# Kernel tuning notes

Measured on AMD Instinct MI355X. Metric: run time of the kernel, lower is better.

Reference implementation:

```python
import jax, jax.numpy as jnp
import numpy as np

NUM_CLASSES = 50000
FEAT_DIM = 256
BATCH = 131072
LAMBDA_CENT = 0.5
EPS = 1e-12  # matches F.normalize default eps


def setup_inputs() -> dict:
    key = jax.random.key(0)
    k1, k2, k3 = jax.random.split(key, 3)
    features = jax.random.normal(k1, (BATCH, FEAT_DIM), dtype=jnp.float32)
    labels = jax.random.randint(k2, (BATCH,), 0, NUM_CLASSES)
    centers = jax.random.normal(k3, (NUM_CLASSES, FEAT_DIM), dtype=jnp.float32)
    return {"features": features, "labels": labels, "centers": centers}


def reference(features, labels, centers):
    # L2 normalize rows (F.normalize, p=2, dim=1)
    norms = jnp.linalg.norm(features, axis=1, keepdims=True)
    f = features / jnp.maximum(norms, EPS)
    # gather centers per sample: [B, D]
    cb = centers[labels]
    loss_cent = jnp.sum((f - cb) ** 2) / features.shape[0]
    # training-mode center update, vectorized:
    # torch loop: delta[labels[i]] += (cb[i] - f[i]) / (1 + count(labels == labels[i]))
    cnt = jax.ops.segment_sum(jnp.ones(labels.shape, f.dtype), labels,
                              num_segments=NUM_CLASSES)  # [C]
    w = 1.0 / (1.0 + cnt[labels])  # [B]
    delta = jax.ops.segment_sum((cb - f) * w[:, None], labels,
                                num_segments=NUM_CLASSES)  # [C, D]
    new_centers = centers - LAMBDA_CENT * delta
    return loss_cent, new_centers
```

## Files before the change

### kernel.cpp

```cpp
#include <hip/hip_runtime.h>
#include <hip/hip_bf16.h>
#include <math.h>

#define BATCH   131072
#define FEAT    256
#define NCLASS  50000
#define EPS     1e-12f
#define LAMBDA  0.5f
#define CAP     32

constexpr int WPB     = 4;
constexpr int NBLK_SS = NCLASS / WPB;
constexpr int NSCAN   = (NCLASS + 255) / 256;


__device__ __forceinline__ float wave_reduce_sum(float v) {
    #pragma unroll
    for (int m = 32; m; m >>= 1) v += __shfl_xor(v, m, 64);
    return v;
}

__global__ __launch_bounds__(256) void histo(const int* __restrict__ labels,
                                             int* __restrict__ cnt) {
    const int i = blockIdx.x * 256 + threadIdx.x;
    atomicAdd(&cnt[labels[i]], 1);
}

__global__ __launch_bounds__(256) void scan_bsum(const int* __restrict__ cnt,
                                                 int* __restrict__ bsum) {
    __shared__ int s[256];
    const int i = blockIdx.x * 256 + threadIdx.x;
    s[threadIdx.x] = (i < NCLASS) ? cnt[i] : 0;
    __syncthreads();
    for (int off = 128; off; off >>= 1) {
        if (threadIdx.x < off) s[threadIdx.x] += s[threadIdx.x + off];
        __syncthreads();
    }
    if (threadIdx.x == 0) bsum[blockIdx.x] = s[0];
}

__global__ __launch_bounds__(256) void scan_boff(const int* __restrict__ bsum,
                                                 int* __restrict__ boff) {
    __shared__ int s[256];
    const int t = threadIdx.x;
    const int v = (t < NSCAN) ? bsum[t] : 0;
    s[t] = v;
    __syncthreads();
    for (int off = 1; off < 256; off <<= 1) {
        int u = (t >= off) ? s[t - off] : 0;
        __syncthreads();
        s[t] += u;
        __syncthreads();
    }
    if (t < NSCAN) boff[t] = s[t] - v;
}

__global__ __launch_bounds__(256) void scan_final(const int* __restrict__ cnt,
                                                  const int* __restrict__ boff,
                                                  int* __restrict__ cursor) {
    __shared__ int s[256];
    const int t = threadIdx.x;
    const int i = blockIdx.x * 256 + t;
    const int v = (i < NCLASS) ? cnt[i] : 0;
    s[t] = v;
    __syncthreads();
    for (int off = 1; off < 256; off <<= 1) {
        int u = (t >= off) ? s[t - off] : 0;
        __syncthreads();
        s[t] += u;
        __syncthreads();
    }
    if (i < NCLASS) cursor[i] = s[t] - v + boff[blockIdx.x];
}

__global__ __launch_bounds__(256) void scatter_idx(const int* __restrict__ labels,
                                                   int* __restrict__ cursor,
                                                   int* __restrict__ sIdx) {
    const int i = blockIdx.x * 256 + threadIdx.x;
    const int slot = atomicAdd(&cursor[labels[i]], 1);
    sIdx[slot] = i;
}

__global__ __launch_bounds__(256) void segsum_gather(
        const float* __restrict__ feat,
        const float* __restrict__ centers,
        const int*   __restrict__ cnt,
        const int*   __restrict__ cursor_end,
        const int*   __restrict__ sIdx,
        float*       __restrict__ outc,
        float*       __restrict__ pB) {
    const int wave = threadIdx.x >> 6;
    const int lane = threadIdx.x & 63;
    const int c    = blockIdx.x * WPB + wave;

    const int n     = cnt[c];
    const int start = cursor_end[c] - n;

    float4 acc   = {0.f, 0.f, 0.f, 0.f};
    float  fsum2 = 0.f;

    for (int base = 0; base < n; base += 64) {
        const int cn = min(64, n - base);
        int myidx = 0;
        if (lane < cn) myidx = sIdx[start + base + lane];

        for (int s = 0; s < cn; s += 4) {
            const int m  = cn - s;
            const int r0 = __shfl(myidx, s + 0, 64);
            const int r1 = __shfl(myidx, s + 1, 64);
            const int r2 = __shfl(myidx, s + 2, 64);
            const int r3 = __shfl(myidx, s + 3, 64);

            const float4 v0 = ((const float4*)(feat + (size_t)r0 * FEAT))[lane];
            float4 v1 = {0.f,0.f,0.f,0.f}, v2 = {0.f,0.f,0.f,0.f}, v3 = {0.f,0.f,0.f,0.f};
            if (m > 1) v1 = ((const float4*)(feat + (size_t)r1 * FEAT))[lane];
            if (m > 2) v2 = ((const float4*)(feat + (size_t)r2 * FEAT))[lane];
            if (m > 3) v3 = ((const float4*)(feat + (size_t)r3 * FEAT))[lane];

            float a0 = v0.x*v0.x + v0.y*v0.y + v0.z*v0.z + v0.w*v0.w;
            float a1 = v1.x*v1.x + v1.y*v1.y + v1.z*v1.z + v1.w*v1.w;
            float a2 = v2.x*v2.x + v2.y*v2.y + v2.z*v2.z + v2.w*v2.w;
            float a3 = v3.x*v3.x + v3.y*v3.y + v3.z*v3.z + v3.w*v3.w;

            #pragma unroll
            for (int sh = 32; sh; sh >>= 1) {
                a0 += __shfl_xor(a0, sh, 64);
                a1 += __shfl_xor(a1, sh, 64);
                a2 += __shfl_xor(a2, sh, 64);
                a3 += __shfl_xor(a3, sh, 64);
            }

            const float i0 = 1.0f / fmaxf(sqrtf(a0), EPS);
            const float i1 = 1.0f / fmaxf(sqrtf(a1), EPS);
            const float i2 = 1.0f / fmaxf(sqrtf(a2), EPS);
            const float i3 = 1.0f / fmaxf(sqrtf(a3), EPS);

            acc.x += v0.x*i0 + v1.x*i1 + v2.x*i2 + v3.x*i3;
            acc.y += v0.y*i0 + v1.y*i1 + v2.y*i2 + v3.y*i3;
            acc.z += v0.z*i0 + v1.z*i1 + v2.z*i2 + v3.z*i3;
            acc.w += v0.w*i0 + v1.w*i1 + v2.w*i2 + v3.w*i3;

            fsum2 += (a0*i0)*i0 + (a1*i1)*i1 + (a2*i2)*i2 + (a3*i3)*i3;
        }
    }

    const float4 cv = ((const float4*)(centers + (size_t)c * FEAT))[lane];
    const float fn = (float)n;
    const float w  = 1.0f / (1.0f + fn);

    float4 nc;
    nc.x = cv.x - LAMBDA * (fn * cv.x - acc.x) * w;
    nc.y = cv.y - LAMBDA * (fn * cv.y - acc.y) * w;
    nc.z = cv.z - LAMBDA * (fn * cv.z - acc.z) * w;
    nc.w = cv.w - LAMBDA * (fn * cv.w - acc.w) * w;
    ((float4*)(outc + (size_t)c * FEAT))[lane] = nc;

    float lp = fn * (cv.x*cv.x + cv.y*cv.y + cv.z*cv.z + cv.w*cv.w)
             - 2.0f * (acc.x*cv.x + acc.y*cv.y + acc.z*cv.z + acc.w*cv.w);
    lp = wave_reduce_sum(lp);

    __shared__ float red[WPB];
    if (lane == 0) red[wave] = lp + fsum2;
    __syncthreads();
    if (threadIdx.x == 0)
        pB[blockIdx.x] = red[0] + red[1] + red[2] + red[3];
}

__global__ __launch_bounds__(1024) void finish(const float* __restrict__ pB,
                                               float* __restrict__ out0) {
    float s = 0.0f;
    for (int i = threadIdx.x; i < NBLK_SS; i += 1024) s += pB[i];
    s = wave_reduce_sum(s);
    __shared__ float red[16];
    const int wave = threadIdx.x >> 6;
    const int lane = threadIdx.x & 63;
    if (lane == 0) red[wave] = s;
    __syncthreads();
    if (threadIdx.x == 0) {
        float t = 0.0f;
        #pragma unroll
        for (int i = 0; i < 16; ++i) t += red[i];
        out0[0] = t * (1.0f / (float)BATCH);
    }
}


__global__ __launch_bounds__(256) void scatter_bucket(const int* __restrict__ labels,
                                                      int* __restrict__ cnt,
                                                      int* __restrict__ bucket) {
    const int i = blockIdx.x * 256 + threadIdx.x;
    const int c = labels[i];
    const int slot = atomicAdd(&cnt[c], 1);
    if (slot < CAP) bucket[c * CAP + slot] = i;
}

__global__ __launch_bounds__(256) void gather_bucket(
        const float* __restrict__ feat, const float* __restrict__ centers,
        const int* __restrict__ cnt, const int* __restrict__ bucket,
        float* __restrict__ outc, float* __restrict__ pB) {
    const int wave = threadIdx.x >> 6;
    const int lane = threadIdx.x & 63;
    const int c    = blockIdx.x * WPB + wave;
    const int n = min(cnt[c], CAP);
    const int myidx = (lane < n) ? bucket[c * CAP + lane] : 0;
    float4 acc = {0.f,0.f,0.f,0.f};
    float fsum2 = 0.f;
    for (int s = 0; s < n; ++s) {
        const int r = __shfl(myidx, s, 64);
        const float4 v = ((const float4*)(feat + (size_t)r * FEAT))[lane];
        float ss = wave_reduce_sum(v.x*v.x + v.y*v.y + v.z*v.z + v.w*v.w);
        const float rinv = 1.0f / fmaxf(sqrtf(ss), EPS);
        acc.x += v.x*rinv; acc.y += v.y*rinv; acc.z += v.z*rinv; acc.w += v.w*rinv;
        fsum2 += ss * rinv * rinv;
    }
    const float4 cv = ((const float4*)(centers + (size_t)c * FEAT))[lane];
    const float fn = (float)n;
    const float w  = 1.0f / (1.0f + fn);
    float4 nc;
    nc.x = cv.x - LAMBDA * (fn*cv.x - acc.x) * w;
    nc.y = cv.y - LAMBDA * (fn*cv.y - acc.y) * w;
    nc.z = cv.z - LAMBDA * (fn*cv.z - acc.z) * w;
    nc.w = cv.w - LAMBDA * (fn*cv.w - acc.w) * w;
    ((float4*)(outc + (size_t)c * FEAT))[lane] = nc;
    float lp = fn * (cv.x*cv.x + cv.y*cv.y + cv.z*cv.z + cv.w*cv.w)
             - 2.0f * (acc.x*cv.x + acc.y*cv.y + acc.z*cv.z + acc.w*cv.w);
    lp = wave_reduce_sum(lp);
    __shared__ float red[WPB];
    if (lane == 0) red[wave] = lp + fsum2;
    __syncthreads();
    if (threadIdx.x == 0)
        pB[blockIdx.x] = red[0] + red[1] + red[2] + red[3];
}

__global__ __launch_bounds__(1024) void finishB(const float* __restrict__ pB,
                                                float* __restrict__ out0) {
    float s = 0.0f;
    for (int i = threadIdx.x; i < NBLK_SS; i += 1024) s += pB[i];
    s = wave_reduce_sum(s);
    __shared__ float red[16];
    const int wave = threadIdx.x >> 6;
    const int lane = threadIdx.x & 63;
    if (lane == 0) red[wave] = s;
    __syncthreads();
    if (threadIdx.x == 0) {
        float t = 0.0f;
        #pragma unroll
        for (int i = 0; i < 16; ++i) t += red[i];
        out0[0] = t * (1.0f / (float)BATCH);
    }
}

extern "C" void kernel_launch(void* const* d_in, const int* in_sizes, int n_in,
                              void* d_out, int out_size, void* d_ws, size_t ws_size,
                              hipStream_t stream) {
    const float* feat    = (const float*)d_in[0];
    const int*   labels  = (const int*)  d_in[1];
    const float* centers = (const float*)d_in[2];
    float* out = (float*)d_out;

    const size_t need_fast = ((size_t)NCLASS * 2 + 512 + NBLK_SS + BATCH) * 4;

    if (ws_size >= need_fast) {
        int*   cnt    = (int*)d_ws;
        int*   cursor = cnt + NCLASS;
        int*   bsum   = cursor + NCLASS;
        int*   boff   = bsum + 256;
        float* pB     = (float*)(boff + 256);
        int*   sIdx   = (int*)(pB + NBLK_SS);

        hipMemsetAsync(cnt, 0, NCLASS * sizeof(int), stream);
        histo      <<<BATCH / 256, 256, 0, stream>>>(labels, cnt);
        scan_bsum  <<<NSCAN, 256, 0, stream>>>(cnt, bsum);
        scan_boff  <<<1, 256, 0, stream>>>(bsum, boff);
        scan_final <<<NSCAN, 256, 0, stream>>>(cnt, boff, cursor);
        scatter_idx<<<BATCH / 256, 256, 0, stream>>>(labels, cursor, sIdx);
        segsum_gather<<<NBLK_SS, 256, 0, stream>>>(feat, centers, cnt, cursor,
                                                   sIdx, out + 1, pB);
        finish<<<1, 1024, 0, stream>>>(pB, out);
    } else {
        int*   cnt    = (int*)d_ws;
        int*   bucket = cnt + NCLASS;
        float* pB     = (float*)(bucket + (size_t)NCLASS * CAP);
        hipMemsetAsync(cnt, 0, NCLASS * sizeof(int), stream);
        scatter_bucket<<<BATCH / 256, 256, 0, stream>>>(labels, cnt, bucket);
        gather_bucket <<<NBLK_SS, 256, 0, stream>>>(feat, centers, cnt, bucket,
                                                    out + 1, pB);
        finishB<<<1, 1024, 0, stream>>>(pB, out);
    }
}
```

Before: 277.7 us.

## Process eight classes per wave over contiguous sorted sample range

Each wave now handles eight consecutive classes, walking their concatenated sorted sample indices as one stream and routing each row's normalized contribution to a per-class accumulator picked by a uniform class index. With about 2.6 samples per class, the old one-class-per-wave loop left most lanes and load slots idle with partial 4-row groups. The new layout packs full 4-row batches across class boundaries, at the cost of eight float4 accumulators per lane, a branchy per-class select, and fewer blocks.

Result: slower. 285.0 us (+2.6%).

```diff
diff --git a/kernel.cpp b/kernel.cpp
--- a/kernel.cpp
+++ b/kernel.cpp
@@ -1,5 +1,4 @@
 #include <hip/hip_runtime.h>
-#include <hip/hip_bf16.h>
 #include <math.h>
 
 #define BATCH   131072
@@ -10,6 +9,9 @@
 #define CAP     32
 
 constexpr int WPB     = 4;
+constexpr int CPW     = 8;
+constexpr int CPB     = WPB * CPW;
+constexpr int NBLK_G  = (NCLASS + CPB - 1) / CPB;
 constexpr int NBLK_SS = NCLASS / WPB;
 constexpr int NSCAN   = (NCLASS + 255) / 256;
 
@@ -81,7 +83,7 @@
     sIdx[slot] = i;
 }
 
-__global__ __launch_bounds__(256) void segsum_gather(
+__global__ __launch_bounds__(256) void segsum_multi(
         const float* __restrict__ feat,
         const float* __restrict__ centers,
         const int*   __restrict__ cnt,
@@ -91,31 +93,48 @@
         float*       __restrict__ pB) {
     const int wave = threadIdx.x >> 6;
     const int lane = threadIdx.x & 63;
-    const int c    = blockIdx.x * WPB + wave;
-
-    const int n     = cnt[c];
-    const int start = cursor_end[c] - n;
-
-    float4 acc   = {0.f, 0.f, 0.f, 0.f};
-    float  fsum2 = 0.f;
-
-    for (int base = 0; base < n; base += 64) {
-        const int cn = min(64, n - base);
+    const int c0   = (blockIdx.x * WPB + wave) * CPW;
+
+    int e[CPW], nn[CPW];
+    #pragma unroll
+    for (int j = 0; j < CPW; ++j) {
+        const int c = c0 + j;
+        e[j]  = (c < NCLASS) ? cursor_end[c] : BATCH;
+        nn[j] = (c < NCLASS) ? cnt[c]        : 0;
+    }
+    const int S = e[0] - nn[0];
+    const int R = e[CPW - 1] - S;
+
+    int B[CPW - 1];
+    #pragma unroll
+    for (int j = 0; j < CPW - 1; ++j) B[j] = e[j] - S;
+
+    float4 acc[CPW];
+    #pragma unroll
+    for (int j = 0; j < CPW; ++j) acc[j] = make_float4(0.f, 0.f, 0.f, 0.f);
+    float fsum2 = 0.f;
+
+    for (int base = 0; base < R; base += 64) {
         int myidx = 0;
-        if (lane < cn) myidx = sIdx[start + base + lane];
-
-        for (int s = 0; s < cn; s += 4) {
-            const int m  = cn - s;
+        int jcls  = 0;
+        if (base + lane < R) myidx = sIdx[S + base + lane];
+        {
+            const int rr = base + lane;
+            #pragma unroll
+            for (int t = 0; t < CPW - 1; ++t) jcls += (rr >= B[t]) ? 1 : 0;
+        }
+        const int gn = min(64, R - base);
+
+        for (int s = 0; s < gn; s += 4) {
             const int r0 = __shfl(myidx, s + 0, 64);
             const int r1 = __shfl(myidx, s + 1, 64);
             const int r2 = __shfl(myidx, s + 2, 64);
             const int r3 = __shfl(myidx, s + 3, 64);
 
             const float4 v0 = ((const float4*)(feat + (size_t)r0 * FEAT))[lane];
-            float4 v1 = {0.f,0.f,0.f,0.f}, v2 = {0.f,0.f,0.f,0.f}, v3 = {0.f,0.f,0.f,0.f};
-            if (m > 1) v1 = ((const float4*)(feat + (size_t)r1 * FEAT))[lane];
-            if (m > 2) v2 = ((const float4*)(feat + (size_t)r2 * FEAT))[lane];
-            if (m > 3) v3 = ((const float4*)(feat + (size_t)r3 * FEAT))[lane];
+            const float4 v1 = ((const float4*)(feat + (size_t)r1 * FEAT))[lane];
+            const float4 v2 = ((const float4*)(feat + (size_t)r2 * FEAT))[lane];
+            const float4 v3 = ((const float4*)(feat + (size_t)r3 * FEAT))[lane];
 
             float a0 = v0.x*v0.x + v0.y*v0.y + v0.z*v0.z + v0.w*v0.w;
             float a1 = v1.x*v1.x + v1.y*v1.y + v1.z*v1.z + v1.w*v1.w;
@@ -123,40 +142,67 @@
             float a3 = v3.x*v3.x + v3.y*v3.y + v3.z*v3.z + v3.w*v3.w;
 
             #pragma unroll
-            for (int sh = 32; sh; sh >>= 1) {
-                a0 += __shfl_xor(a0, sh, 64);
-                a1 += __shfl_xor(a1, sh, 64);
-                a2 += __shfl_xor(a2, sh, 64);
-                a3 += __shfl_xor(a3, sh, 64);
+            for (int m = 32; m; m >>= 1) {
+                a0 += __shfl_xor(a0, m, 64);
+                a1 += __shfl_xor(a1, m, 64);
+                a2 += __shfl_xor(a2, m, 64);
+                a3 += __shfl_xor(a3, m, 64);
             }
 
-            const float i0 = 1.0f / fmaxf(sqrtf(a0), EPS);
-            const float i1 = 1.0f / fmaxf(sqrtf(a1), EPS);
-            const float i2 = 1.0f / fmaxf(sqrtf(a2), EPS);
-            const float i3 = 1.0f / fmaxf(sqrtf(a3), EPS);
-
-            acc.x += v0.x*i0 + v1.x*i1 + v2.x*i2 + v3.x*i3;
-            acc.y += v0.y*i0 + v1.y*i1 + v2.y*i2 + v3.y*i3;
-            acc.z += v0.z*i0 + v1.z*i1 + v2.z*i2 + v3.z*i3;
-            acc.w += v0.w*i0 + v1.w*i1 + v2.w*i2 + v3.w*i3;
+            const int rr = base + s;
+            const float i0 = (rr + 0 < R) ? 1.0f / fmaxf(sqrtf(a0), EPS) : 0.f;
+            const float i1 = (rr + 1 < R) ? 1.0f / fmaxf(sqrtf(a1), EPS) : 0.f;
+            const float i2 = (rr + 2 < R) ? 1.0f / fmaxf(sqrtf(a2), EPS) : 0.f;
+            const float i3 = (rr + 3 < R) ? 1.0f / fmaxf(sqrtf(a3), EPS) : 0.f;
 
             fsum2 += (a0*i0)*i0 + (a1*i1)*i1 + (a2*i2)*i2 + (a3*i3)*i3;
+
+            const int j0 = __builtin_amdgcn_readfirstlane(__shfl(jcls, s + 0, 64));
+            const int j1 = __builtin_amdgcn_readfirstlane(__shfl(jcls, s + 1, 64));
+            const int j2 = __builtin_amdgcn_readfirstlane(__shfl(jcls, s + 2, 64));
+            const int j3 = __builtin_amdgcn_readfirstlane(__shfl(jcls, s + 3, 64));
+
+            #pragma unroll
+            for (int t = 0; t < CPW; ++t) {
+                if (t == j0) { acc[t].x += v0.x*i0; acc[t].y += v0.y*i0;
+                               acc[t].z += v0.z*i0; acc[t].w += v0.w*i0; }
+                if (t == j1) { acc[t].x += v1.x*i1; acc[t].y += v1.y*i1;
+                               acc[t].z += v1.z*i1; acc[t].w += v1.w*i1; }
+                if (t == j2) { acc[t].x += v2.x*i2; acc[t].y += v2.y*i2;
+                               acc[t].z += v2.z*i2; acc[t].w += v2.w*i2; }
+                if (t == j3) { acc[t].x += v3.x*i3; acc[t].y += v3.y*i3;
+                               acc[t].z += v3.z*i3; acc[t].w += v3.w*i3; }
+            }
         }
     }
 
-    const float4 cv = ((const float4*)(centers + (size_t)c * FEAT))[lane];
-    const float fn = (float)n;
-    const float w  = 1.0f / (1.0f + fn);
-
-    float4 nc;
-    nc.x = cv.x - LAMBDA * (fn * cv.x - acc.x) * w;
-    nc.y = cv.y - LAMBDA * (fn * cv.y - acc.y) * w;
-    nc.z = cv.z - LAMBDA * (fn * cv.z - acc.z) * w;
-    nc.w = cv.w - LAMBDA * (fn * cv.w - acc.w) * w;
-    ((float4*)(outc + (size_t)c * FEAT))[lane] = nc;
-
-    float lp = fn * (cv.x*cv.x + cv.y*cv.y + cv.z*cv.z + cv.w*cv.w)
-             - 2.0f * (acc.x*cv.x + acc.y*cv.y + acc.z*cv.z + acc.w*cv.w);
+    float4 cv[CPW];
+    #pragma unroll
+    for (int j = 0; j < CPW; ++j) {
+        const int c = c0 + j;
+        cv[j] = (c < NCLASS)
+              ? ((const float4*)(centers + (size_t)c * FEAT))[lane]
+              : make_float4(0.f, 0.f, 0.f, 0.f);
+    }
+
+    float lp = 0.f;
+    #pragma unroll
+    for (int j = 0; j < CPW; ++j) {
+        const int c  = c0 + j;
+        const float fn = (float)nn[j];
+        const float w  = 1.0f / (1.0f + fn);
+        float4 nc;
+        nc.x = cv[j].x - LAMBDA * (fn * cv[j].x - acc[j].x) * w;
+        nc.y = cv[j].y - LAMBDA * (fn * cv[j].y - acc[j].y) * w;
+        nc.z = cv[j].z - LAMBDA * (fn * cv[j].z - acc[j].z) * w;
+        nc.w = cv[j].w - LAMBDA * (fn * cv[j].w - acc[j].w) * w;
+        if (c < NCLASS)
+            ((float4*)(outc + (size_t)c * FEAT))[lane] = nc;
+        lp += fn * (cv[j].x*cv[j].x + cv[j].y*cv[j].y +
+                    cv[j].z*cv[j].z + cv[j].w*cv[j].w)
+            - 2.0f * (acc[j].x*cv[j].x + acc[j].y*cv[j].y +
+                      acc[j].z*cv[j].z + acc[j].w*cv[j].w);
+    }
     lp = wave_reduce_sum(lp);
 
     __shared__ float red[WPB];
@@ -169,7 +215,7 @@
 __global__ __launch_bounds__(1024) void finish(const float* __restrict__ pB,
                                                float* __restrict__ out0) {
     float s = 0.0f;
-    for (int i = threadIdx.x; i < NBLK_SS; i += 1024) s += pB[i];
+    for (int i = threadIdx.x; i < NBLK_G; i += 1024) s += pB[i];
     s = wave_reduce_sum(s);
     __shared__ float red[16];
     const int wave = threadIdx.x >> 6;
@@ -258,7 +304,8 @@
     const float* centers = (const float*)d_in[2];
     float* out = (float*)d_out;
 
-    const size_t need_fast = ((size_t)NCLASS * 2 + 512 + NBLK_SS + BATCH) * 4;
+    const size_t need_fast =
+        ((size_t)NCLASS * 2 + 512 + NBLK_G + BATCH) * 4;
 
     if (ws_size >= need_fast) {
         int*   cnt    = (int*)d_ws;
@@ -266,7 +313,7 @@
         int*   bsum   = cursor + NCLASS;
         int*   boff   = bsum + 256;
         float* pB     = (float*)(boff + 256);
-        int*   sIdx   = (int*)(pB + NBLK_SS);
+        int*   sIdx   = (int*)(pB + NBLK_G);
 
         hipMemsetAsync(cnt, 0, NCLASS * sizeof(int), stream);
         histo      <<<BATCH / 256, 256, 0, stream>>>(labels, cnt);
@@ -274,8 +321,8 @@
         scan_boff  <<<1, 256, 0, stream>>>(bsum, boff);
         scan_final <<<NSCAN, 256, 0, stream>>>(cnt, boff, cursor);
         scatter_idx<<<BATCH / 256, 256, 0, stream>>>(labels, cursor, sIdx);
-        segsum_gather<<<NBLK_SS, 256, 0, stream>>>(feat, centers, cnt, cursor,
-                                                   sIdx, out + 1, pB);
+        segsum_multi<<<NBLK_G, 256, 0, stream>>>(feat, centers, cnt, cursor,
+                                                 sIdx, out + 1, pB);
         finish<<<1, 1024, 0, stream>>>(pB, out);
     } else {
         int*   cnt    = (int*)d_ws;
```

## Make segment-sum gather persistent with software-prefetched next class metadata

Applied to the files above, without the earlier changes.

Replaces the one-wave-per-class gather kernel with a persistent kernel of 2048 blocks where each wave walks classes with a stride and prefetches the next class's count, index list and center row while processing the current one. Feature rows are loaded eight at a time with masking instead of four with branches, raising memory-level parallelism. The final reduction reads fewer partial sums. The risk is load imbalance across waves from uneven class counts, and always issuing eight loads when classes are small.

Result: no change. 277.8 us, median of 2 (+0.0%).

```diff
diff --git a/kernel.cpp b/kernel.cpp
--- a/kernel.cpp
+++ b/kernel.cpp
@@ -1,5 +1,4 @@
 #include <hip/hip_runtime.h>
-#include <hip/hip_bf16.h>
 #include <math.h>
 
 #define BATCH   131072
@@ -10,6 +9,8 @@
 #define CAP     32
 
 constexpr int WPB     = 4;
+constexpr int PBLK    = 2048;
+constexpr int TOTW    = PBLK * WPB;
 constexpr int NBLK_SS = NCLASS / WPB;
 constexpr int NSCAN   = (NCLASS + 255) / 256;
 
@@ -81,7 +82,67 @@
     sIdx[slot] = i;
 }
 
-__global__ __launch_bounds__(256) void segsum_gather(
+__device__ __forceinline__ void burst8(const float* __restrict__ feat,
+                                       int sidx, int lane, int s, int cc,
+                                       float4& acc, float& fsum2) {
+    const int r0 = __shfl(sidx, s + 0, 64);
+    const int r1 = __shfl(sidx, s + 1, 64);
+    const int r2 = __shfl(sidx, s + 2, 64);
+    const int r3 = __shfl(sidx, s + 3, 64);
+    const int r4 = __shfl(sidx, s + 4, 64);
+    const int r5 = __shfl(sidx, s + 5, 64);
+    const int r6 = __shfl(sidx, s + 6, 64);
+    const int r7 = __shfl(sidx, s + 7, 64);
+
+    const float4 v0 = ((const float4*)(feat + (size_t)r0 * FEAT))[lane];
+    const float4 v1 = ((const float4*)(feat + (size_t)r1 * FEAT))[lane];
+    const float4 v2 = ((const float4*)(feat + (size_t)r2 * FEAT))[lane];
+    const float4 v3 = ((const float4*)(feat + (size_t)r3 * FEAT))[lane];
+    const float4 v4 = ((const float4*)(feat + (size_t)r4 * FEAT))[lane];
+    const float4 v5 = ((const float4*)(feat + (size_t)r5 * FEAT))[lane];
+    const float4 v6 = ((const float4*)(feat + (size_t)r6 * FEAT))[lane];
+    const float4 v7 = ((const float4*)(feat + (size_t)r7 * FEAT))[lane];
+
+    float a0 = v0.x*v0.x + v0.y*v0.y + v0.z*v0.z + v0.w*v0.w;
+    float a1 = v1.x*v1.x + v1.y*v1.y + v1.z*v1.z + v1.w*v1.w;
+    float a2 = v2.x*v2.x + v2.y*v2.y + v2.z*v2.z + v2.w*v2.w;
+    float a3 = v3.x*v3.x + v3.y*v3.y + v3.z*v3.z + v3.w*v3.w;
+    float a4 = v4.x*v4.x + v4.y*v4.y + v4.z*v4.z + v4.w*v4.w;
+    float a5 = v5.x*v5.x + v5.y*v5.y + v5.z*v5.z + v5.w*v5.w;
+    float a6 = v6.x*v6.x + v6.y*v6.y + v6.z*v6.z + v6.w*v6.w;
+    float a7 = v7.x*v7.x + v7.y*v7.y + v7.z*v7.z + v7.w*v7.w;
+
+    #pragma unroll
+    for (int m = 32; m; m >>= 1) {
+        a0 += __shfl_xor(a0, m, 64); a1 += __shfl_xor(a1, m, 64);
+        a2 += __shfl_xor(a2, m, 64); a3 += __shfl_xor(a3, m, 64);
+        a4 += __shfl_xor(a4, m, 64); a5 += __shfl_xor(a5, m, 64);
+        a6 += __shfl_xor(a6, m, 64); a7 += __shfl_xor(a7, m, 64);
+    }
+
+    const float i0 = (s + 0 < cc) ? 1.0f / fmaxf(sqrtf(a0), EPS) : 0.f;
+    const float i1 = (s + 1 < cc) ? 1.0f / fmaxf(sqrtf(a1), EPS) : 0.f;
+    const float i2 = (s + 2 < cc) ? 1.0f / fmaxf(sqrtf(a2), EPS) : 0.f;
+    const float i3 = (s + 3 < cc) ? 1.0f / fmaxf(sqrtf(a3), EPS) : 0.f;
+    const float i4 = (s + 4 < cc) ? 1.0f / fmaxf(sqrtf(a4), EPS) : 0.f;
+    const float i5 = (s + 5 < cc) ? 1.0f / fmaxf(sqrtf(a5), EPS) : 0.f;
+    const float i6 = (s + 6 < cc) ? 1.0f / fmaxf(sqrtf(a6), EPS) : 0.f;
+    const float i7 = (s + 7 < cc) ? 1.0f / fmaxf(sqrtf(a7), EPS) : 0.f;
+
+    acc.x += (v0.x*i0 + v1.x*i1) + (v2.x*i2 + v3.x*i3)
+           + (v4.x*i4 + v5.x*i5) + (v6.x*i6 + v7.x*i7);
+    acc.y += (v0.y*i0 + v1.y*i1) + (v2.y*i2 + v3.y*i3)
+           + (v4.y*i4 + v5.y*i5) + (v6.y*i6 + v7.y*i7);
+    acc.z += (v0.z*i0 + v1.z*i1) + (v2.z*i2 + v3.z*i3)
+           + (v4.z*i4 + v5.z*i5) + (v6.z*i6 + v7.z*i7);
+    acc.w += (v0.w*i0 + v1.w*i1) + (v2.w*i2 + v3.w*i3)
+           + (v4.w*i4 + v5.w*i5) + (v6.w*i6 + v7.w*i7);
+
+    fsum2 += ((a0*i0)*i0 + (a1*i1)*i1) + ((a2*i2)*i2 + (a3*i3)*i3)
+           + ((a4*i4)*i4 + (a5*i5)*i5) + ((a6*i6)*i6 + (a7*i7)*i7);
+}
+
+__global__ __launch_bounds__(256) void segsum_persist(
         const float* __restrict__ feat,
         const float* __restrict__ centers,
         const int*   __restrict__ cnt,
@@ -91,74 +152,112 @@
         float*       __restrict__ pB) {
     const int wave = threadIdx.x >> 6;
     const int lane = threadIdx.x & 63;
-    const int c    = blockIdx.x * WPB + wave;
-
-    const int n     = cnt[c];
-    const int start = cursor_end[c] - n;
-
-    float4 acc   = {0.f, 0.f, 0.f, 0.f};
-    float  fsum2 = 0.f;
-
-    for (int base = 0; base < n; base += 64) {
-        const int cn = min(64, n - base);
-        int myidx = 0;
-        if (lane < cn) myidx = sIdx[start + base + lane];
-
-        for (int s = 0; s < cn; s += 4) {
-            const int m  = cn - s;
-            const int r0 = __shfl(myidx, s + 0, 64);
-            const int r1 = __shfl(myidx, s + 1, 64);
-            const int r2 = __shfl(myidx, s + 2, 64);
-            const int r3 = __shfl(myidx, s + 3, 64);
-
-            const float4 v0 = ((const float4*)(feat + (size_t)r0 * FEAT))[lane];
-            float4 v1 = {0.f,0.f,0.f,0.f}, v2 = {0.f,0.f,0.f,0.f}, v3 = {0.f,0.f,0.f,0.f};
-            if (m > 1) v1 = ((const float4*)(feat + (size_t)r1 * FEAT))[lane];
-            if (m > 2) v2 = ((const float4*)(feat + (size_t)r2 * FEAT))[lane];
-            if (m > 3) v3 = ((const float4*)(feat + (size_t)r3 * FEAT))[lane];
-
+    int c = blockIdx.x * WPB + wave;
+
+    float lp    = 0.f;
+    float fsum2 = 0.f;
+
+    int n  = cnt[c];
+    int st = cursor_end[c] - n;
+    int sidx = (lane < n) ? sIdx[st + lane] : 0;
+    float4 cv = ((const float4*)(centers + (size_t)c * FEAT))[lane];
+
+    while (true) {
+        const int c2 = c + TOTW;
+        int n2 = 0, st2 = 0;
+        if (c2 < NCLASS) { n2 = cnt[c2]; st2 = cursor_end[c2] - n2; }
+
+        const int cn0 = min(n, 64);
+
+        const int r0 = __shfl(sidx, 0, 64);
+        const int r1 = __shfl(sidx, 1, 64);
+        const int r2 = __shfl(sidx, 2, 64);
+        const int r3 = __shfl(sidx, 3, 64);
+        const int r4 = __shfl(sidx, 4, 64);
+        const int r5 = __shfl(sidx, 5, 64);
+        const int r6 = __shfl(sidx, 6, 64);
+        const int r7 = __shfl(sidx, 7, 64);
+        const float4 v0 = ((const float4*)(feat + (size_t)r0 * FEAT))[lane];
+        const float4 v1 = ((const float4*)(feat + (size_t)r1 * FEAT))[lane];
+        const float4 v2 = ((const float4*)(feat + (size_t)r2 * FEAT))[lane];
+        const float4 v3 = ((const float4*)(feat + (size_t)r3 * FEAT))[lane];
+        const float4 v4 = ((const float4*)(feat + (size_t)r4 * FEAT))[lane];
+        const float4 v5 = ((const float4*)(feat + (size_t)r5 * FEAT))[lane];
+        const float4 v6 = ((const float4*)(feat + (size_t)r6 * FEAT))[lane];
+        const float4 v7 = ((const float4*)(feat + (size_t)r7 * FEAT))[lane];
+
+        int sidx2 = 0;
+        float4 cv2 = make_float4(0.f, 0.f, 0.f, 0.f);
+        if (c2 < NCLASS) {
+            if (lane < n2) sidx2 = sIdx[st2 + lane];
+            cv2 = ((const float4*)(centers + (size_t)c2 * FEAT))[lane];
+        }
+
+        float4 acc = {0.f, 0.f, 0.f, 0.f};
+        {
             float a0 = v0.x*v0.x + v0.y*v0.y + v0.z*v0.z + v0.w*v0.w;
             float a1 = v1.x*v1.x + v1.y*v1.y + v1.z*v1.z + v1.w*v1.w;
             float a2 = v2.x*v2.x + v2.y*v2.y + v2.z*v2.z + v2.w*v2.w;
             float a3 = v3.x*v3.x + v3.y*v3.y + v3.z*v3.z + v3.w*v3.w;
-
+            float a4 = v4.x*v4.x + v4.y*v4.y + v4.z*v4.z + v4.w*v4.w;
+            float a5 = v5.x*v5.x + v5.y*v5.y + v5.z*v5.z + v5.w*v5.w;
+            float a6 = v6.x*v6.x + v6.y*v6.y + v6.z*v6.z + v6.w*v6.w;
+            float a7 = v7.x*v7.x + v7.y*v7.y + v7.z*v7.z + v7.w*v7.w;
             #pragma unroll
-            for (int sh = 32; sh; sh >>= 1) {
-                a0 += __shfl_xor(a0, sh, 64);
-                a1 += __shfl_xor(a1, sh, 64);
-                a2 += __shfl_xor(a2, sh, 64);
-                a3 += __shfl_xor(a3, sh, 64);
+            for (int m = 32; m; m >>= 1) {
+                a0 += __shfl_xor(a0, m, 64); a1 += __shfl_xor(a1, m, 64);
+                a2 += __shfl_xor(a2, m, 64); a3 += __shfl_xor(a3, m, 64);
+                a4 += __shfl_xor(a4, m, 64); a5 += __shfl_xor(a5, m, 64);
+                a6 += __shfl_xor(a6, m, 64); a7 += __shfl_xor(a7, m, 64);
             }
-
-            const float i0 = 1.0f / fmaxf(sqrtf(a0), EPS);
-            const float i1 = 1.0f / fmaxf(sqrtf(a1), EPS);
-            const float i2 = 1.0f / fmaxf(sqrtf(a2), EPS);
-            const float i3 = 1.0f / fmaxf(sqrtf(a3), EPS);
-
-            acc.x += v0.x*i0 + v1.x*i1 + v2.x*i2 + v3.x*i3;
-            acc.y += v0.y*i0 + v1.y*i1 + v2.y*i2 + v3.y*i3;
-            acc.z += v0.z*i0 + v1.z*i1 + v2.z*i2 + v3.z*i3;
-            acc.w += v0.w*i0 + v1.w*i1 + v2.w*i2 + v3.w*i3;
-
-            fsum2 += (a0*i0)*i0 + (a1*i1)*i1 + (a2*i2)*i2 + (a3*i3)*i3;
+            const float i0 = (0 < cn0) ? 1.0f / fmaxf(sqrtf(a0), EPS) : 0.f;
+            const float i1 = (1 < cn0) ? 1.0f / fmaxf(sqrtf(a1), EPS) : 0.f;
+            const float i2 = (2 < cn0) ? 1.0f / fmaxf(sqrtf(a2), EPS) : 0.f;
+            const float i3 = (3 < cn0) ? 1.0f / fmaxf(sqrtf(a3), EPS) : 0.f;
+            const float i4 = (4 < cn0) ? 1.0f / fmaxf(sqrtf(a4), EPS) : 0.f;
+            const float i5 = (5 < cn0) ? 1.0f / fmaxf(sqrtf(a5), EPS) : 0.f;
+            const float i6 = (6 < cn0) ? 1.0f / fmaxf(sqrtf(a6), EPS) : 0.f;
+            const float i7 = (7 < cn0) ? 1.0f / fmaxf(sqrtf(a7), EPS) : 0.f;
+
+            acc.x += (v0.x*i0 + v1.x*i1) + (v2.x*i2 + v3.x*i3)
+                   + (v4.x*i4 + v5.x*i5) + (v6.x*i6 + v7.x*i7);
+            acc.y += (v0.y*i0 + v1.y*i1) + (v2.y*i2 + v3.y*i3)
+                   + (v4.y*i4 + v5.y*i5) + (v6.y*i6 + v7.y*i7);
+            acc.z += (v0.z*i0 + v1.z*i1) + (v2.z*i2 + v3.z*i3)
+                   + (v4.z*i4 + v5.z*i5) + (v6.z*i6 + v7.z*i7);
+            acc.w += (v0.w*i0 + v1.w*i1) + (v2.w*i2 + v3.w*i3)
+                   + (v4.w*i4 + v5.w*i5) + (v6.w*i6 + v7.w*i7);
+
+            fsum2 += ((a0*i0)*i0 + (a1*i1)*i1) + ((a2*i2)*i2 + (a3*i3)*i3)
+                   + ((a4*i4)*i4 + (a5*i5)*i5) + ((a6*i6)*i6 + (a7*i7)*i7);
         }
-    }
-
-    const float4 cv = ((const float4*)(centers + (size_t)c * FEAT))[lane];
-    const float fn = (float)n;
-    const float w  = 1.0f / (1.0f + fn);
-
-    float4 nc;
-    nc.x = cv.x - LAMBDA * (fn * cv.x - acc.x) * w;
-    nc.y = cv.y - LAMBDA * (fn * cv.y - acc.y) * w;
-    nc.z = cv.z - LAMBDA * (fn * cv.z - acc.z) * w;
-    nc.w = cv.w - LAMBDA * (fn * cv.w - acc.w) * w;
-    ((float4*)(outc + (size_t)c * FEAT))[lane] = nc;
-
-    float lp = fn * (cv.x*cv.x + cv.y*cv.y + cv.z*cv.z + cv.w*cv.w)
-             - 2.0f * (acc.x*cv.x + acc.y*cv.y + acc.z*cv.z + acc.w*cv.w);
+
+        for (int s = 8; s < cn0; s += 8)
+            burst8(feat, sidx, lane, s, cn0, acc, fsum2);
+        for (int base = 64; base < n; base += 64) {
+            const int cc = min(64, n - base);
+            const int sx = (base + lane < n) ? sIdx[st + base + lane] : 0;
+            for (int s = 0; s < cc; s += 8)
+                burst8(feat, sx, lane, s, cc, acc, fsum2);
+        }
+
+        const float fn = (float)n;
+        const float w  = 1.0f / (1.0f + fn);
+        float4 nc;
+        nc.x = cv.x - LAMBDA * (fn * cv.x - acc.x) * w;
+        nc.y = cv.y - LAMBDA * (fn * cv.y - acc.y) * w;
+        nc.z = cv.z - LAMBDA * (fn * cv.z - acc.z) * w;
+        nc.w = cv.w - LAMBDA * (fn * cv.w - acc.w) * w;
+        ((float4*)(outc + (size_t)c * FEAT))[lane] = nc;
+
+        lp += fn * (cv.x*cv.x + cv.y*cv.y + cv.z*cv.z + cv.w*cv.w)
+            - 2.0f * (acc.x*cv.x + acc.y*cv.y + acc.z*cv.z + acc.w*cv.w);
+
+        if (c2 >= NCLASS) break;
+        c = c2; n = n2; st = st2; sidx = sidx2; cv = cv2;
+    }
+
     lp = wave_reduce_sum(lp);
-
     __shared__ float red[WPB];
     if (lane == 0) red[wave] = lp + fsum2;
     __syncthreads();
@@ -169,7 +268,7 @@
 __global__ __launch_bounds__(1024) void finish(const float* __restrict__ pB,
                                                float* __restrict__ out0) {
     float s = 0.0f;
-    for (int i = threadIdx.x; i < NBLK_SS; i += 1024) s += pB[i];
+    for (int i = threadIdx.x; i < PBLK; i += 1024) s += pB[i];
     s = wave_reduce_sum(s);
     __shared__ float red[16];
     const int wave = threadIdx.x >> 6;
@@ -258,7 +357,8 @@
     const float* centers = (const float*)d_in[2];
     float* out = (float*)d_out;
 
-    const size_t need_fast = ((size_t)NCLASS * 2 + 512 + NBLK_SS + BATCH) * 4;
+    const size_t need_fast =
+        ((size_t)NCLASS * 2 + 512 + PBLK + BATCH) * 4;
 
     if (ws_size >= need_fast) {
         int*   cnt    = (int*)d_ws;
@@ -266,7 +366,7 @@
         int*   bsum   = cursor + NCLASS;
         int*   boff   = bsum + 256;
         float* pB     = (float*)(boff + 256);
-        int*   sIdx   = (int*)(pB + NBLK_SS);
+        int*   sIdx   = (int*)(pB + PBLK);
 
         hipMemsetAsync(cnt, 0, NCLASS * sizeof(int), stream);
         histo      <<<BATCH / 256, 256, 0, stream>>>(labels, cnt);
@@ -274,8 +374,8 @@
         scan_boff  <<<1, 256, 0, stream>>>(bsum, boff);
         scan_final <<<NSCAN, 256, 0, stream>>>(cnt, boff, cursor);
         scatter_idx<<<BATCH / 256, 256, 0, stream>>>(labels, cursor, sIdx);
-        segsum_gather<<<NBLK_SS, 256, 0, stream>>>(feat, centers, cnt, cursor,
-                                                   sIdx, out + 1, pB);
+        segsum_persist<<<PBLK, 256, 0, stream>>>(feat, centers, cnt, cursor,
+                                                 sIdx, out + 1, pB);
         finish<<<1, 1024, 0, stream>>>(pB, out);
     } else {
         int*   cnt    = (int*)d_ws;
```

## Process two classes per wave and fold final reduction into atomics

Applied to the files above, without the earlier changes.

Each wave now handles two adjacent classes by walking their combined contiguous sorted index range, so tiny per-class segments are packed into fuller 4-row load batches. The scan writes a separate exclusive-offset array so segment bounds are read directly. The separate finish kernel is removed; each block atomically adds its scaled partial loss into the output after a memset. This cuts per-wave overhead and one launch, but adds branchy per-row accumulator selection, and the atomic float sum is nondeterministic in order.

New measurement: 295.8 us. 6.5% more time.

```diff
diff --git a/kernel.cpp b/kernel.cpp
--- a/kernel.cpp
+++ b/kernel.cpp
@@ -1,5 +1,4 @@
 #include <hip/hip_runtime.h>
-#include <hip/hip_bf16.h>
 #include <math.h>
 
 #define BATCH   131072
@@ -10,6 +9,8 @@
 #define CAP     32
 
 constexpr int WPB     = 4;
+constexpr int CPW     = 2;
+constexpr int NBLK_G  = NCLASS / (WPB * CPW);
 constexpr int NBLK_SS = NCLASS / WPB;
 constexpr int NSCAN   = (NCLASS + 255) / 256;
 
@@ -57,7 +58,8 @@
 
 __global__ __launch_bounds__(256) void scan_final(const int* __restrict__ cnt,
                                                   const int* __restrict__ boff,
-                                                  int* __restrict__ cursor) {
+                                                  int* __restrict__ cursor,
+                                                  int* __restrict__ cursEx) {
     __shared__ int s[256];
     const int t = threadIdx.x;
     const int i = blockIdx.x * 256 + t;
@@ -70,7 +72,12 @@
         s[t] += u;
         __syncthreads();
     }
-    if (i < NCLASS) cursor[i] = s[t] - v + boff[blockIdx.x];
+    if (i < NCLASS) {
+        const int start = s[t] - v + boff[blockIdx.x];
+        cursor[i] = start;
+        cursEx[i] = start;
+        if (i == NCLASS - 1) cursEx[NCLASS] = start + v;
+    }
 }
 
 __global__ __launch_bounds__(256) void scatter_idx(const int* __restrict__ labels,
@@ -81,31 +88,37 @@
     sIdx[slot] = i;
 }
 
-__global__ __launch_bounds__(256) void segsum_gather(
+__global__ __launch_bounds__(256) void segsum2(
         const float* __restrict__ feat,
         const float* __restrict__ centers,
-        const int*   __restrict__ cnt,
-        const int*   __restrict__ cursor_end,
+        const int*   __restrict__ cursEx,
         const int*   __restrict__ sIdx,
         float*       __restrict__ outc,
-        float*       __restrict__ pB) {
+        float*       __restrict__ out0) {
     const int wave = threadIdx.x >> 6;
     const int lane = threadIdx.x & 63;
-    const int c    = blockIdx.x * WPB + wave;
-
-    const int n     = cnt[c];
-    const int start = cursor_end[c] - n;
-
-    float4 acc   = {0.f, 0.f, 0.f, 0.f};
+    const int c0   = (blockIdx.x * WPB + wave) * CPW;
+
+    const int2 ee = *(const int2*)(cursEx + c0);
+    const int  e2 = cursEx[c0 + 2];
+    const int  S  = ee.x;
+    const int  B0 = ee.y - ee.x;
+    const int  R  = e2 - ee.x;
+
+    const float4 cv0 = ((const float4*)(centers + (size_t)(c0 + 0) * FEAT))[lane];
+    const float4 cv1 = ((const float4*)(centers + (size_t)(c0 + 1) * FEAT))[lane];
+
+    float4 acc0 = {0.f, 0.f, 0.f, 0.f};
+    float4 acc1 = {0.f, 0.f, 0.f, 0.f};
     float  fsum2 = 0.f;
 
-    for (int base = 0; base < n; base += 64) {
-        const int cn = min(64, n - base);
+    for (int base = 0; base < R; base += 64) {
+        const int cn = min(64, R - base);
         int myidx = 0;
-        if (lane < cn) myidx = sIdx[start + base + lane];
+        if (lane < cn) myidx = sIdx[S + base + lane];
 
         for (int s = 0; s < cn; s += 4) {
-            const int m  = cn - s;
+            const int m = cn - s;
             const int r0 = __shfl(myidx, s + 0, 64);
             const int r1 = __shfl(myidx, s + 1, 64);
             const int r2 = __shfl(myidx, s + 2, 64);
@@ -123,65 +136,69 @@
             float a3 = v3.x*v3.x + v3.y*v3.y + v3.z*v3.z + v3.w*v3.w;
 
             #pragma unroll
-            for (int sh = 32; sh; sh >>= 1) {
-                a0 += __shfl_xor(a0, sh, 64);
-                a1 += __shfl_xor(a1, sh, 64);
-                a2 += __shfl_xor(a2, sh, 64);
-                a3 += __shfl_xor(a3, sh, 64);
+            for (int mm = 32; mm; mm >>= 1) {
+                a0 += __shfl_xor(a0, mm, 64);
+                a1 += __shfl_xor(a1, mm, 64);
+                a2 += __shfl_xor(a2, mm, 64);
+                a3 += __shfl_xor(a3, mm, 64);
             }
 
-            const float i0 = 1.0f / fmaxf(sqrtf(a0), EPS);
-            const float i1 = 1.0f / fmaxf(sqrtf(a1), EPS);
-            const float i2 = 1.0f / fmaxf(sqrtf(a2), EPS);
-            const float i3 = 1.0f / fmaxf(sqrtf(a3), EPS);
-
-            acc.x += v0.x*i0 + v1.x*i1 + v2.x*i2 + v3.x*i3;
-            acc.y += v0.y*i0 + v1.y*i1 + v2.y*i2 + v3.y*i3;
-            acc.z += v0.z*i0 + v1.z*i1 + v2.z*i2 + v3.z*i3;
-            acc.w += v0.w*i0 + v1.w*i1 + v2.w*i2 + v3.w*i3;
+            const int rr = base + s;
+            const float i0 = (rr + 0 < R) ? 1.0f / fmaxf(sqrtf(a0), EPS) : 0.f;
+            const float i1 = (rr + 1 < R) ? 1.0f / fmaxf(sqrtf(a1), EPS) : 0.f;
+            const float i2 = (rr + 2 < R) ? 1.0f / fmaxf(sqrtf(a2), EPS) : 0.f;
+            const float i3 = (rr + 3 < R) ? 1.0f / fmaxf(sqrtf(a3), EPS) : 0.f;
 
             fsum2 += (a0*i0)*i0 + (a1*i1)*i1 + (a2*i2)*i2 + (a3*i3)*i3;
+
+            if (rr + 0 >= B0) { acc1.x += v0.x*i0; acc1.y += v0.y*i0;
+                                acc1.z += v0.z*i0; acc1.w += v0.w*i0; }
+            else              { acc0.x += v0.x*i0; acc0.y += v0.y*i0;
+                                acc0.z += v0.z*i0; acc0.w += v0.w*i0; }
+            if (rr + 1 >= B0) { acc1.x += v1.x*i1; acc1.y += v1.y*i1;
+                                acc1.z += v1.z*i1; acc1.w += v1.w*i1; }
+            else              { acc0.x += v1.x*i1; acc0.y += v1.y*i1;
+                                acc0.z += v1.z*i1; acc0.w += v1.w*i1; }
+            if (rr + 2 >= B0) { acc1.x += v2.x*i2; acc1.y += v2.y*i2;
+                                acc1.z += v2.z*i2; acc1.w += v2.w*i2; }
+            else              { acc0.x += v2.x*i2; acc0.y += v2.y*i2;
+                                acc0.z += v2.z*i2; acc0.w += v2.w*i2; }
+            if (rr + 3 >= B0) { acc1.x += v3.x*i3; acc1.y += v3.y*i3;
+                                acc1.z += v3.z*i3; acc1.w += v3.w*i3; }
+            else              { acc0.x += v3.x*i3; acc0.y += v3.y*i3;
+                                acc0.z += v3.z*i3; acc0.w += v3.w*i3; }
         }
     }
 
-    const float4 cv = ((const float4*)(centers + (size_t)c * FEAT))[lane];
-    const float fn = (float)n;
-    const float w  = 1.0f / (1.0f + fn);
+    const float fn0 = (float)B0;
+    const float fn1 = (float)(R - B0);
+    const float w0  = 1.0f / (1.0f + fn0);
+    const float w1  = 1.0f / (1.0f + fn1);
 
     float4 nc;
-    nc.x = cv.x - LAMBDA * (fn * cv.x - acc.x) * w;
-    nc.y = cv.y - LAMBDA * (fn * cv.y - acc.y) * w;
-    nc.z = cv.z - LAMBDA * (fn * cv.z - acc.z) * w;
-    nc.w = cv.w - LAMBDA * (fn * cv.w - acc.w) * w;
-    ((float4*)(outc + (size_t)c * FEAT))[lane] = nc;
-
-    float lp = fn * (cv.x*cv.x + cv.y*cv.y + cv.z*cv.z + cv.w*cv.w)
-             - 2.0f * (acc.x*cv.x + acc.y*cv.y + acc.z*cv.z + acc.w*cv.w);
+    nc.x = cv0.x - LAMBDA * (fn0 * cv0.x - acc0.x) * w0;
+    nc.y = cv0.y - LAMBDA * (fn0 * cv0.y - acc0.y) * w0;
+    nc.z = cv0.z - LAMBDA * (fn0 * cv0.z - acc0.z) * w0;
+    nc.w = cv0.w - LAMBDA * (fn0 * cv0.w - acc0.w) * w0;
+    ((float4*)(outc + (size_t)(c0 + 0) * FEAT))[lane] = nc;
+
+    nc.x = cv1.x - LAMBDA * (fn1 * cv1.x - acc1.x) * w1;
+    nc.y = cv1.y - LAMBDA * (fn1 * cv1.y - acc1.y) * w1;
+    nc.z = cv1.z - LAMBDA * (fn1 * cv1.z - acc1.z) * w1;
+    nc.w = cv1.w - LAMBDA * (fn1 * cv1.w - acc1.w) * w1;
+    ((float4*)(outc + (size_t)(c0 + 1) * FEAT))[lane] = nc;
+
+    float lp = fn0 * (cv0.x*cv0.x + cv0.y*cv0.y + cv0.z*cv0.z + cv0.w*cv0.w)
+             - 2.0f * (acc0.x*cv0.x + acc0.y*cv0.y + acc0.z*cv0.z + acc0.w*cv0.w)
+             + fn1 * (cv1.x*cv1.x + cv1.y*cv1.y + cv1.z*cv1.z + cv1.w*cv1.w)
+             - 2.0f * (acc1.x*cv1.x + acc1.y*cv1.y + acc1.z*cv1.z + acc1.w*cv1.w);
     lp = wave_reduce_sum(lp);
 
     __shared__ float red[WPB];
     if (lane == 0) red[wave] = lp + fsum2;
     __syncthreads();
     if (threadIdx.x == 0)
-        pB[blockIdx.x] = red[0] + red[1] + red[2] + red[3];
-}
-
-__global__ __launch_bounds__(1024) void finish(const float* __restrict__ pB,
-                                               float* __restrict__ out0) {
-    float s = 0.0f;
-    for (int i = threadIdx.x; i < NBLK_SS; i += 1024) s += pB[i];
-    s = wave_reduce_sum(s);
-    __shared__ float red[16];
-    const int wave = threadIdx.x >> 6;
-    const int lane = threadIdx.x & 63;
-    if (lane == 0) red[wave] = s;
-    __syncthreads();
-    if (threadIdx.x == 0) {
-        float t = 0.0f;
-        #pragma unroll
-        for (int i = 0; i < 16; ++i) t += red[i];
-        out0[0] = t * (1.0f / (float)BATCH);
-    }
+        atomicAdd(out0, (red[0] + red[1] + red[2] + red[3]) * (1.0f / (float)BATCH));
 }
 
 
@@ -258,25 +275,26 @@
     const float* centers = (const float*)d_in[2];
     float* out = (float*)d_out;
 
-    const size_t need_fast = ((size_t)NCLASS * 2 + 512 + NBLK_SS + BATCH) * 4;
+    const size_t need_fast =
+        ((size_t)NCLASS * 3 + 1 + 512 + BATCH) * 4;
 
     if (ws_size >= need_fast) {
-        int*   cnt    = (int*)d_ws;
-        int*   cursor = cnt + NCLASS;
-        int*   bsum   = cursor + NCLASS;
-        int*   boff   = bsum + 256;
-        float* pB     = (float*)(boff + 256);
-        int*   sIdx   = (int*)(pB + NBLK_SS);
+        int* cnt    = (int*)d_ws;
+        int* cursor = cnt + NCLASS;
+        int* cursEx = cursor + NCLASS;
+        int* bsum   = cursEx + NCLASS + 1;
+        int* boff   = bsum + 256;
+        int* sIdx   = boff + 256;
 
         hipMemsetAsync(cnt, 0, NCLASS * sizeof(int), stream);
+        hipMemsetAsync(out, 0, sizeof(float), stream);
         histo      <<<BATCH / 256, 256, 0, stream>>>(labels, cnt);
         scan_bsum  <<<NSCAN, 256, 0, stream>>>(cnt, bsum);
         scan_boff  <<<1, 256, 0, stream>>>(bsum, boff);
-        scan_final <<<NSCAN, 256, 0, stream>>>(cnt, boff, cursor);
+        scan_final <<<NSCAN, 256, 0, stream>>>(cnt, boff, cursor, cursEx);
         scatter_idx<<<BATCH / 256, 256, 0, stream>>>(labels, cursor, sIdx);
-        segsum_gather<<<NBLK_SS, 256, 0, stream>>>(feat, centers, cnt, cursor,
-                                                   sIdx, out + 1, pB);
-        finish<<<1, 1024, 0, stream>>>(pB, out);
+        segsum2    <<<NBLK_G, 256, 0, stream>>>(feat, centers, cursEx, sIdx,
+                                                out + 1, out);
     } else {
         int*   cnt    = (int*)d_ws;
         int*   bucket = cnt + NCLASS;
```
